# Performance work log

Hardware: AMD Instinct MI355X
Metric: run time of the kernel (lower is better)

The kernel has to match this reference:

```python
import jax, jax.numpy as jnp
import numpy as np

TEMPERATURE = 0.2
EPS = 1e-12  # F.normalize clamp eps


def setup_inputs() -> dict:
    key = jax.random.key(0)
    k1, k2 = jax.random.split(key)
    N, D = 4096, 256
    Z_1 = jax.random.normal(k1, (N, D), dtype=jnp.float32)
    Z_2 = jax.random.normal(k2, (N, D), dtype=jnp.float32)
    return {"Z_1": Z_1, "Z_2": Z_2}


def reference(Z_1, Z_2):
    N = Z_1.shape[0]
    M = 2 * N
    # concat views and L2-normalize rows (torch F.normalize semantics)
    Z = jnp.concatenate([Z_1, Z_2], axis=0)  # [2N, D]
    Z = Z / jnp.maximum(jnp.linalg.norm(Z, axis=1, keepdims=True), EPS)
    # full similarity matrix [2N, 2N]
    sim = jnp.matmul(Z, Z.T) / TEMPERATURE
    # positive for row i is column (i + N) mod 2N (other view of same sample,
    # identity diagonal discarded as in create_contrastive_masks)
    idx = jnp.arange(M)
    pos = sim[idx, (idx + N) % M]  # [2N]
    # logits = [pos, negatives]; label = 0 => CE = logsumexp(pos U negs) - pos.
    # pos U negs = all columns except the identity diagonal.
    diag = idx[:, None] == idx[None, :]
    sim_masked = jnp.where(diag, -jnp.inf, sim)
    lse = jax.nn.logsumexp(sim_masked, axis=1)  # [2N]
    return jnp.mean(lse - pos)
```

## Files before the change

kernel.cpp:

```cpp
#include <hip/hip_runtime.h>
#include <cstdint>
#include <cstddef>

#define TINV 5.0f
#define C5L2E 7.2134752044448170f
#define NROWS 4096
#define DDIM 256
#define MM 8192

typedef __bf16 bf16x8 __attribute__((ext_vector_type(8)));
typedef int i32x4 __attribute__((ext_vector_type(4)));
typedef float f32x4 __attribute__((ext_vector_type(4)));

typedef const void __attribute__((address_space(1)))* gas_ptr;
typedef void __attribute__((address_space(3)))* las_ptr;

__global__ __launch_bounds__(256, 2)
void nrm_kernel(const float* __restrict__ Z1, const float* __restrict__ Z2,
                unsigned short* __restrict__ Zb, float* __restrict__ rowsumAcc) {
    if (blockIdx.x < 32) rowsumAcc[blockIdx.x * 256 + threadIdx.x] = 0.f;
    const int w = threadIdx.x >> 6, lane = threadIdx.x & 63;
    const int row = blockIdx.x * 4 + w;
    const float* src = row < NROWS ? Z1 + (size_t)row * DDIM
                                   : Z2 + (size_t)(row - NROWS) * DDIM;
    float4 v = reinterpret_cast<const float4*>(src)[lane];
    float ss = v.x*v.x + v.y*v.y + v.z*v.z + v.w*v.w;
    #pragma unroll
    for (int m = 1; m < 64; m <<= 1) ss += __shfl_xor(ss, m, 64);
    float inv = 1.0f / fmaxf(sqrtf(ss), 1e-12f);
    float o[4] = { v.x*inv, v.y*inv, v.z*inv, v.w*inv };
    unsigned short us[4];
    #pragma unroll
    for (int e = 0; e < 4; ++e) {
        unsigned int b = __builtin_bit_cast(unsigned int, o[e]);
        b += 0x7FFFu + ((b >> 16) & 1u);
        us[e] = (unsigned short)(b >> 16);
    }
    reinterpret_cast<ushort4*>(Zb + (size_t)row * DDIM)[lane] =
        *reinterpret_cast<ushort4*>(us);
}

__device__ __forceinline__ void stage32(const unsigned short* Zb, char* ldsdst,
                                        int rowStart, int tid) {
    const char* base = reinterpret_cast<const char*>(Zb) + (size_t)rowStart * 512;
    #pragma unroll
    for (int it = 0; it < 8; ++it) {
        int L = it * 4096 + tid * 16;
        int row = L >> 9;
        int soff = row * 512 + ((L & 511) ^ ((row & 15) << 4));
        __builtin_amdgcn_global_load_lds((gas_ptr)(base + soff), (las_ptr)(ldsdst + L),
                                         16, 0, 0);
    }
}

__global__ __launch_bounds__(256, 2)
void sim_lse_kernel(const unsigned short* __restrict__ Zb,
                    float* __restrict__ rowsumAcc,
                    float* __restrict__ posArr) {
    __shared__ char lds[65536];
    __shared__ float colPartLds[4][8][32];
    const int tid = threadIdx.x;
    const int lane = tid & 63;
    const int w = tid >> 6;
    const int wr = w >> 1, wc = w & 1;
    const int r15 = lane & 15, hi = lane >> 4;
    const int r = blockIdx.x >> 3;
    const int s = blockIdx.x & 7;
    const int e0 = r & 7, e1 = e0 ^ 4;
    const int nt = 8 + ((s == e0) || (s == e1));
    const int extraHalf = (s == e1) ? 1 : 0;
    const int R0 = r * 128;

    if (s == 0 && lane < 32) {
        colPartLds[w][0][lane] = 0.f;
        colPartLds[w][1][lane] = 0.f;
    }

    int koff[8];
    #pragma unroll
    for (int kk = 0; kk < 8; ++kk)
        koff[kk] = ((hi << 4) | (kk << 6)) ^ (r15 << 4);

    stage32(Zb, lds, R0, tid);
    stage32(Zb, lds + 32768, R0 + 64, tid);
    __syncthreads();
    i32x4 qf[4][8];
    {
        const char* ab = lds + (wr << 15);
        #pragma unroll
        for (int mf = 0; mf < 4; ++mf)
            #pragma unroll
            for (int kk = 0; kk < 8; ++kk)
                qf[mf][kk] = *reinterpret_cast<const i32x4*>(
                    ab + (mf * 16 + r15) * 512 + koff[kk]);
    }
    __syncthreads();

    int baddr[8];
    #pragma unroll
    for (int kk = 0; kk < 8; ++kk)
        baddr[kk] = (wc * 32 + r15) * 512 + koff[kk];

    float rowsum[4][4] = {{0,0,0,0},{0,0,0,0},{0,0,0,0},{0,0,0,0}};
    const int iBase = R0 + wr * 64 + (hi << 2);

    auto colOf = [&](int t) -> int {
        int d = (t < 8) ? (s + ((t >> 1) << 3)) : 32;
        int half = (t < 8) ? (t & 1) : extraHalf;
        return ((r + d) & 63) * 128 + half * 64;
    };

    stage32(Zb, lds, colOf(0), tid);

    for (int t = 0; t < nt; ++t) {
        const int C0 = colOf(t);
        const int cur = (t & 1) << 15;
        if (t < nt - 1) {
            stage32(Zb, lds + (cur ^ 32768), colOf(t + 1), tid);
            asm volatile("s_waitcnt vmcnt(8)" ::: "memory");
        } else {
            asm volatile("s_waitcnt vmcnt(0)" ::: "memory");
        }
        __builtin_amdgcn_s_barrier();
        __builtin_amdgcn_sched_barrier(0);

        const int mode = (t == 8) ? 2 : ((s == 0 && t < 2) ? 1 : 0);
        #pragma unroll
        for (int nf = 0; nf < 2; ++nf) {
            f32x4 acc[4] = {{0,0,0,0},{0,0,0,0},{0,0,0,0},{0,0,0,0}};
            #pragma unroll
            for (int kk = 0; kk < 8; ++kk) {
                i32x4 b = *reinterpret_cast<const i32x4*>(lds + cur + nf * 8192 + baddr[kk]);
                #pragma unroll
                for (int mf = 0; mf < 4; ++mf)
                    asm("v_mfma_f32_16x16x32_bf16 %0, %1, %2, %0"
                        : "+v"(acc[mf]) : "a"(qf[mf][kk]), "v"(b));
            }
            const int j = C0 + wc * 32 + nf * 16 + r15;
            if (mode == 0) {
                float s8 = 0.f;
                #pragma unroll
                for (int mf = 0; mf < 4; ++mf)
                    #pragma unroll
                    for (int rr = 0; rr < 4; ++rr) {
                        float e = __builtin_amdgcn_exp2f(fmaf(acc[mf][rr], C5L2E, -C5L2E));
                        rowsum[mf][rr] += e;
                        s8 += e;
                    }
                s8 += __shfl_xor(s8, 16, 64);
                s8 += __shfl_xor(s8, 32, 64);
                if (hi == 0) colPartLds[w][t][nf * 16 + r15] = s8;
            } else if (mode == 1) {
                #pragma unroll
                for (int mf = 0; mf < 4; ++mf)
                    #pragma unroll
                    for (int rr = 0; rr < 4; ++rr) {
                        const int i = iBase + mf * 16 + rr;
                        if (j != i)
                            rowsum[mf][rr] += __builtin_amdgcn_exp2f(fmaf(acc[mf][rr], C5L2E, -C5L2E));
                    }
            } else {
                #pragma unroll
                for (int mf = 0; mf < 4; ++mf)
                    #pragma unroll
                    for (int rr = 0; rr < 4; ++rr) {
                        const int i = iBase + mf * 16 + rr;
                        rowsum[mf][rr] += __builtin_amdgcn_exp2f(fmaf(acc[mf][rr], C5L2E, -C5L2E));
                        if (j == (i ^ 4096)) posArr[i] = acc[mf][rr] * TINV;
                    }
            }
        }
        asm volatile("" ::: "memory");
        __builtin_amdgcn_sched_barrier(0);
        __builtin_amdgcn_s_barrier();
    }

    __syncthreads();
    #pragma unroll
    for (int z = 0; z < 2; ++z) {
        const int idx = z * 256 + tid;
        const int tt = idx >> 6, c = idx & 63;
        const int ww = c >> 5;
        float v = colPartLds[ww][tt][c & 31] + colPartLds[2 + ww][tt][c & 31];
        if (v != 0.f) atomicAdd(&rowsumAcc[colOf(tt) + c], v);
    }

    #pragma unroll
    for (int mf = 0; mf < 4; ++mf)
        #pragma unroll
        for (int rr = 0; rr < 4; ++rr) {
            float v = rowsum[mf][rr];
            v += __shfl_xor(v, 1, 64);
            v += __shfl_xor(v, 2, 64);
            v += __shfl_xor(v, 4, 64);
            v += __shfl_xor(v, 8, 64);
            if (r15 == 0) atomicAdd(&rowsumAcc[iBase + mf * 16 + rr], v);
        }
}

__global__ __launch_bounds__(128)
void fin1_kernel(const float* __restrict__ rowsumAcc, const float* __restrict__ posArr,
                 float* __restrict__ blockSums) {
    const int tid = threadIdx.x;
    const int i = blockIdx.x * 128 + tid;
    double v = (double)(logf(rowsumAcc[i]) + 5.0f - posArr[i]);
    #pragma unroll
    for (int m = 1; m < 64; m <<= 1) v += __shfl_xor(v, m, 64);
    __shared__ double red[2];
    if ((tid & 63) == 0) red[tid >> 6] = v;
    __syncthreads();
    if (tid == 0) blockSums[blockIdx.x] = (float)(red[0] + red[1]);
}

__global__ __launch_bounds__(64)
void fin2_kernel(const float* __restrict__ blockSums, float* __restrict__ out) {
    double v = (double)blockSums[threadIdx.x];
    #pragma unroll
    for (int m = 1; m < 64; m <<= 1) v += __shfl_xor(v, m, 64);
    if (threadIdx.x == 0) out[0] = (float)(v / (double)MM);
}

extern "C" void kernel_launch(void* const* d_in, const int* in_sizes, int n_in,
                              void* d_out, int out_size, void* d_ws, size_t ws_size,
                              hipStream_t stream) {
    const float* Z1 = (const float*)d_in[0];
    const float* Z2 = (const float*)d_in[1];
    float* out = (float*)d_out;
    char* ws = (char*)d_ws;
    unsigned short* Zb = (unsigned short*)ws;
    float* posArr = (float*)(ws + 4194304);
    float* rowsumAcc = (float*)(ws + 4194304 + 32768);
    float* blockSums = (float*)(ws + 4194304 + 65536);

    nrm_kernel<<<MM / 4, 256, 0, stream>>>(Z1, Z2, Zb, rowsumAcc);
    sim_lse_kernel<<<64 * 8, 256, 0, stream>>>(Zb, rowsumAcc, posArr);
    fin1_kernel<<<64, 128, 0, stream>>>(rowsumAcc, posArr, blockSums);
    fin2_kernel<<<1, 64, 0, stream>>>(blockSums, out);
}
```

Baseline: 42.53 us.

## Batch LDS B-fragment loads per half-tile and merge finalize kernels into one

The main loop now loads all eight B fragments for each 16-column half before issuing its MFMAs. Both halves' MFMAs run before either epilogue, so LDS latency and exp work are decoupled from the matrix ops, at the cost of more live VGPRs. The two finalize kernels are merged into a single 1024-thread block that reduces all 8192 rows, which removes one kernel launch.

```diff
diff --git a/kernel.cpp b/kernel.cpp
--- a/kernel.cpp
+++ b/kernel.cpp
@@ -110,6 +110,41 @@
         return ((r + d) & 63) * 128 + half * 64;
     };
 
+    auto epi = [&](const f32x4 (&a)[4], int j, int t, int nf, int mode) {
+        if (mode == 0) {
+            float s8 = 0.f;
+            #pragma unroll
+            for (int mf = 0; mf < 4; ++mf)
+                #pragma unroll
+                for (int rr = 0; rr < 4; ++rr) {
+                    float e = __builtin_amdgcn_exp2f(fmaf(a[mf][rr], C5L2E, -C5L2E));
+                    rowsum[mf][rr] += e;
+                    s8 += e;
+                }
+            s8 += __shfl_xor(s8, 16, 64);
+            s8 += __shfl_xor(s8, 32, 64);
+            if (hi == 0) colPartLds[w][t][nf * 16 + r15] = s8;
+        } else if (mode == 1) {
+            #pragma unroll
+            for (int mf = 0; mf < 4; ++mf)
+                #pragma unroll
+                for (int rr = 0; rr < 4; ++rr) {
+                    const int i = iBase + mf * 16 + rr;
+                    if (j != i)
+                        rowsum[mf][rr] += __builtin_amdgcn_exp2f(fmaf(a[mf][rr], C5L2E, -C5L2E));
+                }
+        } else {
+            #pragma unroll
+            for (int mf = 0; mf < 4; ++mf)
+                #pragma unroll
+                for (int rr = 0; rr < 4; ++rr) {
+                    const int i = iBase + mf * 16 + rr;
+                    rowsum[mf][rr] += __builtin_amdgcn_exp2f(fmaf(a[mf][rr], C5L2E, -C5L2E));
+                    if (j == (i ^ 4096)) posArr[i] = a[mf][rr] * TINV;
+                }
+        }
+    };
+
     stage32(Zb, lds, colOf(0), tid);
 
     for (int t = 0; t < nt; ++t) {
@@ -125,51 +160,36 @@
         __builtin_amdgcn_sched_barrier(0);
 
         const int mode = (t == 8) ? 2 : ((s == 0 && t < 2) ? 1 : 0);
-        #pragma unroll
-        for (int nf = 0; nf < 2; ++nf) {
-            f32x4 acc[4] = {{0,0,0,0},{0,0,0,0},{0,0,0,0},{0,0,0,0}};
-            #pragma unroll
-            for (int kk = 0; kk < 8; ++kk) {
-                i32x4 b = *reinterpret_cast<const i32x4*>(lds + cur + nf * 8192 + baddr[kk]);
+
+        f32x4 acc0[4] = {{0,0,0,0},{0,0,0,0},{0,0,0,0},{0,0,0,0}};
+        f32x4 acc1[4] = {{0,0,0,0},{0,0,0,0},{0,0,0,0},{0,0,0,0}};
+        {
+            i32x4 b0[8];
+            #pragma unroll
+            for (int kk = 0; kk < 8; ++kk)
+                b0[kk] = *reinterpret_cast<const i32x4*>(lds + cur + baddr[kk]);
+            #pragma unroll
+            for (int kk = 0; kk < 8; ++kk)
                 #pragma unroll
                 for (int mf = 0; mf < 4; ++mf)
                     asm("v_mfma_f32_16x16x32_bf16 %0, %1, %2, %0"
-                        : "+v"(acc[mf]) : "a"(qf[mf][kk]), "v"(b));
-            }
-            const int j = C0 + wc * 32 + nf * 16 + r15;
-            if (mode == 0) {
-                float s8 = 0.f;
+                        : "+v"(acc0[mf]) : "a"(qf[mf][kk]), "v"(b0[kk]));
+        }
+        {
+            i32x4 b1[8];
+            #pragma unroll
+            for (int kk = 0; kk < 8; ++kk)
+                b1[kk] = *reinterpret_cast<const i32x4*>(lds + cur + 8192 + baddr[kk]);
+            #pragma unroll
+            for (int kk = 0; kk < 8; ++kk)
                 #pragma unroll
                 for (int mf = 0; mf < 4; ++mf)
-                    #pragma unroll
-                    for (int rr = 0; rr < 4; ++rr) {
-                        float e = __builtin_amdgcn_exp2f(fmaf(acc[mf][rr], C5L2E, -C5L2E));
-                        rowsum[mf][rr] += e;
-                        s8 += e;
-                    }
-                s8 += __shfl_xor(s8, 16, 64);
-                s8 += __shfl_xor(s8, 32, 64);
-                if (hi == 0) colPartLds[w][t][nf * 16 + r15] = s8;
-            } else if (mode == 1) {
-                #pragma unroll
-                for (int mf = 0; mf < 4; ++mf)
-                    #pragma unroll
-                    for (int rr = 0; rr < 4; ++rr) {
-                        const int i = iBase + mf * 16 + rr;
-                        if (j != i)
-                            rowsum[mf][rr] += __builtin_amdgcn_exp2f(fmaf(acc[mf][rr], C5L2E, -C5L2E));
-                    }
-            } else {
-                #pragma unroll
-                for (int mf = 0; mf < 4; ++mf)
-                    #pragma unroll
-                    for (int rr = 0; rr < 4; ++rr) {
-                        const int i = iBase + mf * 16 + rr;
-                        rowsum[mf][rr] += __builtin_amdgcn_exp2f(fmaf(acc[mf][rr], C5L2E, -C5L2E));
-                        if (j == (i ^ 4096)) posArr[i] = acc[mf][rr] * TINV;
-                    }
-            }
-        }
+                    asm("v_mfma_f32_16x16x32_bf16 %0, %1, %2, %0"
+                        : "+v"(acc1[mf]) : "a"(qf[mf][kk]), "v"(b1[kk]));
+        }
+        epi(acc0, C0 + wc * 32 + r15, t, 0, mode);
+        epi(acc1, C0 + wc * 32 + 16 + r15, t, 1, mode);
+
         asm volatile("" ::: "memory");
         __builtin_amdgcn_sched_barrier(0);
         __builtin_amdgcn_s_barrier();
@@ -198,26 +218,27 @@
         }
 }
 
-__global__ __launch_bounds__(128)
-void fin1_kernel(const float* __restrict__ rowsumAcc, const float* __restrict__ posArr,
-                 float* __restrict__ blockSums) {
+__global__ __launch_bounds__(1024)
+void fin_kernel(const float* __restrict__ rowsumAcc, const float* __restrict__ posArr,
+                float* __restrict__ out) {
     const int tid = threadIdx.x;
-    const int i = blockIdx.x * 128 + tid;
-    double v = (double)(logf(rowsumAcc[i]) + 5.0f - posArr[i]);
+    double v = 0.0;
+    #pragma unroll
+    for (int z = 0; z < 8; ++z) {
+        const int i = z * 1024 + tid;
+        v += (double)(logf(rowsumAcc[i]) + 5.0f - posArr[i]);
+    }
     #pragma unroll
     for (int m = 1; m < 64; m <<= 1) v += __shfl_xor(v, m, 64);
-    __shared__ double red[2];
+    __shared__ double red[16];
     if ((tid & 63) == 0) red[tid >> 6] = v;
     __syncthreads();
-    if (tid == 0) blockSums[blockIdx.x] = (float)(red[0] + red[1]);
-}
-
-__global__ __launch_bounds__(64)
-void fin2_kernel(const float* __restrict__ blockSums, float* __restrict__ out) {
-    double v = (double)blockSums[threadIdx.x];
-    #pragma unroll
-    for (int m = 1; m < 64; m <<= 1) v += __shfl_xor(v, m, 64);
-    if (threadIdx.x == 0) out[0] = (float)(v / (double)MM);
+    if (tid == 0) {
+        double s = 0.0;
+        #pragma unroll
+        for (int k = 0; k < 16; ++k) s += red[k];
+        out[0] = (float)(s / (double)MM);
+    }
 }
 
 extern "C" void kernel_launch(void* const* d_in, const int* in_sizes, int n_in,
@@ -230,10 +251,8 @@
     unsigned short* Zb = (unsigned short*)ws;
     float* posArr = (float*)(ws + 4194304);
     float* rowsumAcc = (float*)(ws + 4194304 + 32768);
-    float* blockSums = (float*)(ws + 4194304 + 65536);
 
     nrm_kernel<<<MM / 4, 256, 0, stream>>>(Z1, Z2, Zb, rowsumAcc);
     sim_lse_kernel<<<64 * 8, 256, 0, stream>>>(Zb, rowsumAcc, posArr);
-    fin1_kernel<<<64, 128, 0, stream>>>(rowsumAcc, posArr, blockSums);
-    fin2_kernel<<<1, 64, 0, stream>>>(blockSums, out);
-}
+    fin_kernel<<<1, 1024, 0, stream>>>(rowsumAcc, posArr, out);
+}
```

Result: slower. 47.28 us (+11.2%).
